# Performance work log

Measured on AMD Instinct MI355X. Metric: run time of the kernel, lower is better.

## Reference

```python
import jax, jax.numpy as jnp
import numpy as np

KERNEL_LAM = 0.1


def setup_inputs() -> dict:
    key = jax.random.key(0)
    k1, k2, k3, k4 = jax.random.split(key, 4)
    B, H, L, C = 4, 1024, 4096, 1
    u = jax.random.normal(k1, (B, H, L), dtype=jnp.float32)
    kernel = jax.random.normal(k2, (C, H, 2 * L), dtype=jnp.float32) * 0.002
    D = jax.random.normal(k3, (C, H), dtype=jnp.float32)
    W = jax.random.normal(k4, (2 * H, C * H), dtype=jnp.float32) * (1.0 / np.sqrt(C * H))
    b = jnp.zeros((2 * H,), dtype=jnp.float32)
    return {"u": u, "kernel": kernel, "D": D, "W": W, "b": b}


def reference(u, kernel, D, W, b):
    B, H, L = u.shape
    n = 2 * L  # FFT length (kernel is length 2L)
    # soft-threshold the kernel
    k = jax.nn.relu(jnp.abs(kernel) - KERNEL_LAM) * jnp.sign(kernel)  # (C,H,2L)
    # FFT-based long convolution (flashfftconv equivalent): causal conv, take first L
    kf = jnp.fft.rfft(k, n=n)                       # (C,H,n//2+1)
    uf = jnp.fft.rfft(u, n=n)                       # (B,H,n//2+1)
    y = jnp.fft.irfft(uf[:, None] * kf[None], n=n)[..., :L]  # (B,C,H,L)
    # skip connection with D
    y = y + jnp.einsum('bhl,ch->bchl', u, D)
    # (B, C*H, L)
    y = y.reshape(B, -1, L)
    y = jax.nn.silu(y)
    # GLU projection over channel dim
    z = jnp.swapaxes(y, -1, -2) @ W.T + b           # (B,L,2H)
    a, g = jnp.split(z, 2, axis=-1)
    out = a * jax.nn.sigmoid(g)                     # (B,L,H)
    return jnp.swapaxes(out, -1, -2)                # (B,H,L)
```

## Files before the change

kernel.cpp:

```cpp
#include <hip/hip_runtime.h>
#include <stdint.h>

#define HD   1024
#define LD   4096
#define BATCH 4
#define KLEN 8192
#define LAM  0.1f
#define TAP_CAP 65536

typedef __attribute__((ext_vector_type(8))) short short8x;
typedef __attribute__((ext_vector_type(4))) float float4x;

struct Tap { int hd; float v; };

__device__ inline unsigned short f2bf(float x) {
    union { float f; uint32_t u; } v; v.f = x;
    uint32_t u = v.u;
    u += 0x7fffu + ((u >> 16) & 1u);
    return (unsigned short)(u >> 16);
}

__device__ inline void gload16(const void* g, void* l) {
    __builtin_amdgcn_global_load_lds(
        (const __attribute__((address_space(1))) void*)g,
        (__attribute__((address_space(3))) void*)l,
        16, 0, 0);
}

__device__ inline float silu_f(float x) { return x / (1.0f + __expf(-x)); }

__global__ void k_prep(const float* __restrict__ kern, int* __restrict__ ntaps,
                       Tap* __restrict__ taps,
                       const float* __restrict__ W, unsigned short* __restrict__ Wbf) {
    if (blockIdx.x < 1024) {
        int i = blockIdx.x * 256 + threadIdx.x;
        const float4* w4 = (const float4*)W;
        float4 a = w4[i * 2], b = w4[i * 2 + 1];
        short8x o;
        o[0] = (short)f2bf(a.x); o[1] = (short)f2bf(a.y);
        o[2] = (short)f2bf(a.z); o[3] = (short)f2bf(a.w);
        o[4] = (short)f2bf(b.x); o[5] = (short)f2bf(b.y);
        o[6] = (short)f2bf(b.z); o[7] = (short)f2bf(b.w);
        *(short8x*)(Wbf + (int64_t)i * 8) = o;
        return;
    }
    int bid = blockIdx.x - 1024;
    const float4* k4 = (const float4*)kern;
    int64_t total4 = (int64_t)HD * KLEN / 4;
    int64_t stride = (int64_t)2048 * 256;
    for (int64_t i = (int64_t)bid * 256 + threadIdx.x; i < total4; i += stride) {
        float4 v = k4[i];
        float vals[4] = {v.x, v.y, v.z, v.w};
#pragma unroll
        for (int j = 0; j < 4; j++) {
            float a = fabsf(vals[j]) - LAM;
            if (a > 0.0f) {
                int e = (int)(i * 4 + j);
                int slot = atomicAdd(ntaps, 1);
                if (slot < TAP_CAP) { taps[slot].hd = e; taps[slot].v = copysignf(a, vals[j]); }
            }
        }
    }
}

__global__ void k_conv(const float* __restrict__ u, const float* __restrict__ Dv,
                       const int* __restrict__ ntaps_p, const Tap* __restrict__ taps,
                       float* __restrict__ yfull) {
    int nt = *ntaps_p;
    if (nt == 0) return;
    nt = min(nt, TAP_CAP);
    int64_t total = (int64_t)BATCH * HD * LD;
    int64_t stride = (int64_t)gridDim.x * blockDim.x;
    for (int64_t i = (int64_t)blockIdx.x * blockDim.x + threadIdx.x; i < total; i += stride) {
        int t = (int)(i & (LD - 1));
        int64_t bh = i >> 12;
        int h = (int)(bh & (HD - 1));
        float acc = u[i] * Dv[h];
        for (int j = 0; j < nt; j++) {
            int hd = taps[j].hd;
            if ((hd >> 13) != h) continue;
            int d = hd & (KLEN - 1);
            int s;
            if (d <= t) s = t - d;
            else { s = t - d + KLEN; if (s >= LD) continue; }
            acc += taps[j].v * u[(bh << 12) + s];
        }
        yfull[i] = acc;
    }
}

__global__ __launch_bounds__(256) void k_vt(const float* __restrict__ u,
                                            const float* __restrict__ Dv,
                                            const float* __restrict__ yfull,
                                            const int* __restrict__ ntaps_p,
                                            unsigned short* __restrict__ Vt) {
    __shared__ float T[64 * 65];
    int nt = *ntaps_p;
    int lt = blockIdx.x * 64;
    int ht = blockIdx.y * 64;
    int b  = blockIdx.z;
    int tid = threadIdx.x;
    int lq = tid & 15;
    int hh = tid >> 4;
#pragma unroll
    for (int r = 0; r < 4; r++) {
        int h = hh + r * 16;
        int hg = ht + h;
        int64_t base = ((int64_t)b * HD + hg) * LD + lt + lq * 4;
        float4 v;
        if (nt == 0) {
            v = *(const float4*)(u + base);
            float d = Dv[hg];
            v.x *= d; v.y *= d; v.z *= d; v.w *= d;
        } else {
            v = *(const float4*)(yfull + base);
        }
        int p = h * 65 + lq * 4;
        T[p]     = silu_f(v.x);
        T[p + 1] = silu_f(v.y);
        T[p + 2] = silu_f(v.z);
        T[p + 3] = silu_f(v.w);
    }
    __syncthreads();
    int h8 = (tid & 7) * 8;
    int nb = tid >> 3;
#pragma unroll
    for (int p = 0; p < 2; p++) {
        int nl = nb + p * 32;
        short8x o;
#pragma unroll
        for (int j = 0; j < 8; j++) o[j] = (short)f2bf(T[(h8 + j) * 65 + nl]);
        int64_t n = (int64_t)b * LD + lt + nl;
        *(short8x*)(Vt + n * HD + ht + h8) = o;
    }
}

__global__ __launch_bounds__(256, 2) void k_gemm(const unsigned short* __restrict__ Wbf,
                                                 const unsigned short* __restrict__ Vt,
                                                 const float* __restrict__ bvec,
                                                 float* __restrict__ out) {
    __shared__ unsigned short smem[12288];
    int f   = blockIdx.x;
    int xcd = f & 7;
    int s   = f >> 3;
    int ngrp = xcd * 16 + (s & 15);
    int mgrp = s >> 4;
    int m0 = mgrp * 128;
    int n0 = ngrp * 128;
    int tid = threadIdx.x;

    const unsigned short* gsrc[6];
    unsigned short* ldst[6];
#pragma unroll
    for (int i = 0; i < 6; i++) {
        int c = tid + i * 256;
        ldst[i] = smem + c * 8;
        if (c < 1024) {
            int r = c >> 2, slot = c & 3;
            int kg = slot ^ (r & 3);
            int grow = (r < 128) ? (m0 + r) : (1024 + m0 + (r - 128));
            gsrc[i] = Wbf + (int64_t)grow * HD + kg * 8;
        } else {
            int cc = c - 1024;
            int col = cc >> 2, slot = cc & 3;
            int kg = slot ^ (col & 3);
            gsrc[i] = Vt + (int64_t)(n0 + col) * HD + kg * 8;
        }
    }

    int lane = tid & 63;
    int wid  = tid >> 6;
    int wm = wid >> 1, wn = wid & 1;
    int l15 = lane & 15, quad = lane >> 4;
    int kq = quad ^ (l15 & 3);

    int aoff[4], goff[4], boff[4];
#pragma unroll
    for (int i = 0; i < 4; i++) {
        int ra = wm * 64 + i * 16 + l15;
        aoff[i] = ra * 32 + kq * 8;
        goff[i] = (128 + ra) * 32 + kq * 8;
        int cb = wn * 64 + i * 16 + l15;
        boff[i] = 8192 + cb * 32 + kq * 8;
    }

    float4x acca[4][4], accg[4][4];
#pragma unroll
    for (int i = 0; i < 4; i++)
#pragma unroll
        for (int j = 0; j < 4; j++) {
            acca[i][j] = (float4x){0.f, 0.f, 0.f, 0.f};
            accg[i][j] = (float4x){0.f, 0.f, 0.f, 0.f};
        }

    for (int kt = 0; kt < 32; kt++) {
#pragma unroll
        for (int i = 0; i < 6; i++) gload16(gsrc[i], ldst[i]);
#pragma unroll
        for (int i = 0; i < 6; i++) gsrc[i] += 32;
        __syncthreads();
        short8x af[4], gf[4], bf[4];
#pragma unroll
        for (int i = 0; i < 4; i++) {
            af[i] = *(const short8x*)(smem + aoff[i]);
            gf[i] = *(const short8x*)(smem + goff[i]);
            bf[i] = *(const short8x*)(smem + boff[i]);
        }
#pragma unroll
        for (int i = 0; i < 4; i++)
#pragma unroll
            for (int j = 0; j < 4; j++) {
                acca[i][j] = __builtin_amdgcn_mfma_f32_16x16x32_bf16(af[i], bf[j], acca[i][j], 0, 0, 0);
                accg[i][j] = __builtin_amdgcn_mfma_f32_16x16x32_bf16(gf[i], bf[j], accg[i][j], 0, 0, 0);
            }
        __syncthreads();
    }

    int b = n0 >> 12;
#pragma unroll
    for (int i = 0; i < 4; i++) {
        int h = m0 + wm * 64 + i * 16 + quad * 4;
        float ba[4], bg[4];
#pragma unroll
        for (int r = 0; r < 4; r++) { ba[r] = bvec[h + r]; bg[r] = bvec[1024 + h + r]; }
#pragma unroll
        for (int j = 0; j < 4; j++) {
            int n = n0 + wn * 64 + j * 16 + l15;
            int l = n & (LD - 1);
            float* op = out + ((int64_t)b * HD + h) * LD + l;
#pragma unroll
            for (int r = 0; r < 4; r++) {
                float av = acca[i][j][r] + ba[r];
                float gv = accg[i][j][r] + bg[r];
                op[(int64_t)r * LD] = av / (1.0f + __expf(-gv));
            }
        }
    }
}

extern "C" void kernel_launch(void* const* d_in, const int* in_sizes, int n_in,
                              void* d_out, int out_size, void* d_ws, size_t ws_size,
                              hipStream_t stream) {
    const float* u    = (const float*)d_in[0];
    const float* kern = (const float*)d_in[1];
    const float* Dv   = (const float*)d_in[2];
    const float* W    = (const float*)d_in[3];
    const float* bv   = (const float*)d_in[4];
    float* out = (float*)d_out;

    char* ws = (char*)d_ws;
    int* ntaps = (int*)ws;
    Tap* taps  = (Tap*)(ws + 256);
    unsigned short* Wbf = (unsigned short*)(ws + (1 << 20));
    unsigned short* Vt  = (unsigned short*)(ws + (8 << 20));
    float* yfull = (float*)(ws + (40 << 20));

    hipMemsetAsync(ntaps, 0, 256, stream);
    hipLaunchKernelGGL(k_prep, dim3(3072),      dim3(256), 0, stream, kern, ntaps, taps, W, (unsigned short*)Wbf);
    hipLaunchKernelGGL(k_conv, dim3(512),       dim3(256), 0, stream, u, Dv, ntaps, taps, yfull);
    hipLaunchKernelGGL(k_vt,   dim3(64, 16, 4), dim3(256), 0, stream, u, Dv, yfull, ntaps, Vt);
    hipLaunchKernelGGL(k_gemm, dim3(1024),      dim3(256), 0, stream, Wbf, Vt, bv, out);
}
```

Before: 233.8 us.

## Load GEMM MFMA operands directly from global memory instead of LDS staging

The GLU GEMM kernel stops staging W and V tiles through shared memory with global_load_lds and barriers. Each lane now reads its bf16 fragments straight from global memory, and the k-loop is fully unrolled. The block-to-tile mapping also changes from an XCD-aware swizzle to a simple m-fastest order. This removes the LDS round trip and the barrier synchronisation, at the cost of redundant global and L2 traffic, since tiles are no longer shared across waves, and of possibly worse latency hiding. The yfull workspace offset is moved as well.

```diff
diff --git a/kernel.cpp b/kernel.cpp
--- a/kernel.cpp
+++ b/kernel.cpp
@@ -18,13 +18,6 @@
     uint32_t u = v.u;
     u += 0x7fffu + ((u >> 16) & 1u);
     return (unsigned short)(u >> 16);
-}
-
-__device__ inline void gload16(const void* g, void* l) {
-    __builtin_amdgcn_global_load_lds(
-        (const __attribute__((address_space(1))) void*)g,
-        (__attribute__((address_space(3))) void*)l,
-        16, 0, 0);
 }
 
 __device__ inline float silu_f(float x) { return x / (1.0f + __expf(-x)); }
@@ -139,49 +132,26 @@
                                                  const unsigned short* __restrict__ Vt,
                                                  const float* __restrict__ bvec,
                                                  float* __restrict__ out) {
-    __shared__ unsigned short smem[12288];
-    int f   = blockIdx.x;
-    int xcd = f & 7;
-    int s   = f >> 3;
-    int ngrp = xcd * 16 + (s & 15);
-    int mgrp = s >> 4;
+    int mgrp = blockIdx.x & 7;
+    int ngrp = blockIdx.x >> 3;
     int m0 = mgrp * 128;
     int n0 = ngrp * 128;
     int tid = threadIdx.x;
-
-    const unsigned short* gsrc[6];
-    unsigned short* ldst[6];
-#pragma unroll
-    for (int i = 0; i < 6; i++) {
-        int c = tid + i * 256;
-        ldst[i] = smem + c * 8;
-        if (c < 1024) {
-            int r = c >> 2, slot = c & 3;
-            int kg = slot ^ (r & 3);
-            int grow = (r < 128) ? (m0 + r) : (1024 + m0 + (r - 128));
-            gsrc[i] = Wbf + (int64_t)grow * HD + kg * 8;
-        } else {
-            int cc = c - 1024;
-            int col = cc >> 2, slot = cc & 3;
-            int kg = slot ^ (col & 3);
-            gsrc[i] = Vt + (int64_t)(n0 + col) * HD + kg * 8;
-        }
-    }
-
     int lane = tid & 63;
     int wid  = tid >> 6;
     int wm = wid >> 1, wn = wid & 1;
     int l15 = lane & 15, quad = lane >> 4;
-    int kq = quad ^ (l15 & 3);
-
-    int aoff[4], goff[4], boff[4];
+
+    const short8x* pa[4];
+    const short8x* pg[4];
+    const short8x* pb[4];
 #pragma unroll
     for (int i = 0; i < 4; i++) {
-        int ra = wm * 64 + i * 16 + l15;
-        aoff[i] = ra * 32 + kq * 8;
-        goff[i] = (128 + ra) * 32 + kq * 8;
-        int cb = wn * 64 + i * 16 + l15;
-        boff[i] = 8192 + cb * 32 + kq * 8;
+        int ra = m0 + wm * 64 + i * 16 + l15;
+        pa[i] = (const short8x*)(Wbf + (uint32_t)ra * 1024u + quad * 8);
+        pg[i] = (const short8x*)(Wbf + (uint32_t)(ra + 1024) * 1024u + quad * 8);
+        int nb = n0 + wn * 64 + i * 16 + l15;
+        pb[i] = (const short8x*)(Vt + (uint32_t)nb * 1024u + quad * 8);
     }
 
     float4x acca[4][4], accg[4][4];
@@ -193,18 +163,14 @@
             accg[i][j] = (float4x){0.f, 0.f, 0.f, 0.f};
         }
 
+#pragma unroll
     for (int kt = 0; kt < 32; kt++) {
-#pragma unroll
-        for (int i = 0; i < 6; i++) gload16(gsrc[i], ldst[i]);
-#pragma unroll
-        for (int i = 0; i < 6; i++) gsrc[i] += 32;
-        __syncthreads();
         short8x af[4], gf[4], bf[4];
 #pragma unroll
         for (int i = 0; i < 4; i++) {
-            af[i] = *(const short8x*)(smem + aoff[i]);
-            gf[i] = *(const short8x*)(smem + goff[i]);
-            bf[i] = *(const short8x*)(smem + boff[i]);
+            af[i] = pa[i][kt * 4];
+            gf[i] = pg[i][kt * 4];
+            bf[i] = pb[i][kt * 4];
         }
 #pragma unroll
         for (int i = 0; i < 4; i++)
@@ -213,7 +179,6 @@
                 acca[i][j] = __builtin_amdgcn_mfma_f32_16x16x32_bf16(af[i], bf[j], acca[i][j], 0, 0, 0);
                 accg[i][j] = __builtin_amdgcn_mfma_f32_16x16x32_bf16(gf[i], bf[j], accg[i][j], 0, 0, 0);
             }
-        __syncthreads();
     }
 
     int b = n0 >> 12;
@@ -253,10 +218,10 @@
     Tap* taps  = (Tap*)(ws + 256);
     unsigned short* Wbf = (unsigned short*)(ws + (1 << 20));
     unsigned short* Vt  = (unsigned short*)(ws + (8 << 20));
-    float* yfull = (float*)(ws + (40 << 20));
+    float* yfull = (float*)(ws + (48 << 20));
 
     hipMemsetAsync(ntaps, 0, 256, stream);
-    hipLaunchKernelGGL(k_prep, dim3(3072),      dim3(256), 0, stream, kern, ntaps, taps, W, (unsigned short*)Wbf);
+    hipLaunchKernelGGL(k_prep, dim3(3072),      dim3(256), 0, stream, kern, ntaps, taps, W, Wbf);
     hipLaunchKernelGGL(k_conv, dim3(512),       dim3(256), 0, stream, u, Dv, ntaps, taps, yfull);
     hipLaunchKernelGGL(k_vt,   dim3(64, 16, 4), dim3(256), 0, stream, u, Dv, yfull, ntaps, Vt);
     hipLaunchKernelGGL(k_gemm, dim3(1024),      dim3(256), 0, stream, Wbf, Vt, bv, out);
```

After: 336.6 us. 1.44x slower.

## Fuse sparse tap convolution into transpose kernel and deepen GEMM K-tile

Applied to the files above, without the earlier changes.

Removes the separate k_conv kernel and its full fp32 yfull buffer, folding the sparse tap convolution directly into the k_vt transpose/SiLU kernel. This avoids an extra write and read of the activation tensor plus a kernel launch. The GEMM now stages a K-tile of 64 instead of 32, using 8-way XOR swizzling and halving the number of barrier iterations. Its grid becomes a plain 2D mapping without the XCD-aware remap. The larger LDS footprint (48KB) may reduce occupancy, and dropping the XCD remap may hurt L2 locality.

```diff
diff --git a/kernel.cpp b/kernel.cpp
--- a/kernel.cpp
+++ b/kernel.cpp
@@ -63,36 +63,10 @@
     }
 }
 
-__global__ void k_conv(const float* __restrict__ u, const float* __restrict__ Dv,
-                       const int* __restrict__ ntaps_p, const Tap* __restrict__ taps,
-                       float* __restrict__ yfull) {
-    int nt = *ntaps_p;
-    if (nt == 0) return;
-    nt = min(nt, TAP_CAP);
-    int64_t total = (int64_t)BATCH * HD * LD;
-    int64_t stride = (int64_t)gridDim.x * blockDim.x;
-    for (int64_t i = (int64_t)blockIdx.x * blockDim.x + threadIdx.x; i < total; i += stride) {
-        int t = (int)(i & (LD - 1));
-        int64_t bh = i >> 12;
-        int h = (int)(bh & (HD - 1));
-        float acc = u[i] * Dv[h];
-        for (int j = 0; j < nt; j++) {
-            int hd = taps[j].hd;
-            if ((hd >> 13) != h) continue;
-            int d = hd & (KLEN - 1);
-            int s;
-            if (d <= t) s = t - d;
-            else { s = t - d + KLEN; if (s >= LD) continue; }
-            acc += taps[j].v * u[(bh << 12) + s];
-        }
-        yfull[i] = acc;
-    }
-}
-
 __global__ __launch_bounds__(256) void k_vt(const float* __restrict__ u,
                                             const float* __restrict__ Dv,
-                                            const float* __restrict__ yfull,
                                             const int* __restrict__ ntaps_p,
+                                            const Tap* __restrict__ taps,
                                             unsigned short* __restrict__ Vt) {
     __shared__ float T[64 * 65];
     int nt = *ntaps_p;
@@ -107,13 +81,26 @@
         int h = hh + r * 16;
         int hg = ht + h;
         int64_t base = ((int64_t)b * HD + hg) * LD + lt + lq * 4;
-        float4 v;
-        if (nt == 0) {
-            v = *(const float4*)(u + base);
-            float d = Dv[hg];
-            v.x *= d; v.y *= d; v.z *= d; v.w *= d;
-        } else {
-            v = *(const float4*)(yfull + base);
+        float4 v = *(const float4*)(u + base);
+        float d = Dv[hg];
+        v.x *= d; v.y *= d; v.z *= d; v.w *= d;
+        if (nt != 0) {
+            int ncl = min(nt, TAP_CAP);
+            float acc[4] = {v.x, v.y, v.z, v.w};
+            const float* ub = u + ((int64_t)b * HD + hg) * LD;
+            for (int j = 0; j < ncl; j++) {
+                int hd = taps[j].hd;
+                if ((hd >> 13) != hg) continue;
+                int dly = hd & (KLEN - 1);
+#pragma unroll
+                for (int e = 0; e < 4; e++) {
+                    int t = lt + lq * 4 + e;
+                    int s = t - dly;
+                    if (s < 0) s += KLEN;
+                    if (s < LD) acc[e] += taps[j].v * ub[s];
+                }
+            }
+            v.x = acc[0]; v.y = acc[1]; v.z = acc[2]; v.w = acc[3];
         }
         int p = h * 65 + lq * 4;
         T[p]     = silu_f(v.x);
@@ -139,31 +126,26 @@
                                                  const unsigned short* __restrict__ Vt,
                                                  const float* __restrict__ bvec,
                                                  float* __restrict__ out) {
-    __shared__ unsigned short smem[12288];
-    int f   = blockIdx.x;
-    int xcd = f & 7;
-    int s   = f >> 3;
-    int ngrp = xcd * 16 + (s & 15);
-    int mgrp = s >> 4;
-    int m0 = mgrp * 128;
-    int n0 = ngrp * 128;
+    __shared__ unsigned short smem[24576];
+    int m0 = blockIdx.x * 128;
+    int n0 = blockIdx.y * 128;
     int tid = threadIdx.x;
 
-    const unsigned short* gsrc[6];
-    unsigned short* ldst[6];
-#pragma unroll
-    for (int i = 0; i < 6; i++) {
+    const unsigned short* gsrc[12];
+    unsigned short* ldst[12];
+#pragma unroll
+    for (int i = 0; i < 12; i++) {
         int c = tid + i * 256;
         ldst[i] = smem + c * 8;
-        if (c < 1024) {
-            int r = c >> 2, slot = c & 3;
-            int kg = slot ^ (r & 3);
+        if (c < 2048) {
+            int r = c >> 3, s = c & 7;
+            int kg = s ^ (r & 7);
             int grow = (r < 128) ? (m0 + r) : (1024 + m0 + (r - 128));
             gsrc[i] = Wbf + (int64_t)grow * HD + kg * 8;
         } else {
-            int cc = c - 1024;
-            int col = cc >> 2, slot = cc & 3;
-            int kg = slot ^ (col & 3);
+            int cc = c - 2048;
+            int col = cc >> 3, s = cc & 7;
+            int kg = s ^ (col & 7);
             gsrc[i] = Vt + (int64_t)(n0 + col) * HD + kg * 8;
         }
     }
@@ -172,16 +154,16 @@
     int wid  = tid >> 6;
     int wm = wid >> 1, wn = wid & 1;
     int l15 = lane & 15, quad = lane >> 4;
-    int kq = quad ^ (l15 & 3);
-
-    int aoff[4], goff[4], boff[4];
+    int xr = l15 & 7;
+
+    int rba[4], rbg[4], rbb[4];
 #pragma unroll
     for (int i = 0; i < 4; i++) {
         int ra = wm * 64 + i * 16 + l15;
-        aoff[i] = ra * 32 + kq * 8;
-        goff[i] = (128 + ra) * 32 + kq * 8;
+        rba[i] = ra * 64;
+        rbg[i] = (128 + ra) * 64;
         int cb = wn * 64 + i * 16 + l15;
-        boff[i] = 8192 + cb * 32 + kq * 8;
+        rbb[i] = 16384 + cb * 64;
     }
 
     float4x acca[4][4], accg[4][4];
@@ -193,26 +175,30 @@
             accg[i][j] = (float4x){0.f, 0.f, 0.f, 0.f};
         }
 
-    for (int kt = 0; kt < 32; kt++) {
-#pragma unroll
-        for (int i = 0; i < 6; i++) gload16(gsrc[i], ldst[i]);
-#pragma unroll
-        for (int i = 0; i < 6; i++) gsrc[i] += 32;
+    for (int kt = 0; kt < 16; kt++) {
+#pragma unroll
+        for (int i = 0; i < 12; i++) gload16(gsrc[i], ldst[i]);
+#pragma unroll
+        for (int i = 0; i < 12; i++) gsrc[i] += 64;
         __syncthreads();
-        short8x af[4], gf[4], bf[4];
-#pragma unroll
-        for (int i = 0; i < 4; i++) {
-            af[i] = *(const short8x*)(smem + aoff[i]);
-            gf[i] = *(const short8x*)(smem + goff[i]);
-            bf[i] = *(const short8x*)(smem + boff[i]);
-        }
-#pragma unroll
-        for (int i = 0; i < 4; i++)
-#pragma unroll
-            for (int j = 0; j < 4; j++) {
-                acca[i][j] = __builtin_amdgcn_mfma_f32_16x16x32_bf16(af[i], bf[j], acca[i][j], 0, 0, 0);
-                accg[i][j] = __builtin_amdgcn_mfma_f32_16x16x32_bf16(gf[i], bf[j], accg[i][j], 0, 0, 0);
-            }
+#pragma unroll
+        for (int ks = 0; ks < 2; ks++) {
+            int off = ((ks * 4 + quad) ^ xr) * 8;
+            short8x af[4], gf[4], bf[4];
+#pragma unroll
+            for (int i = 0; i < 4; i++) {
+                af[i] = *(const short8x*)(smem + rba[i] + off);
+                gf[i] = *(const short8x*)(smem + rbg[i] + off);
+                bf[i] = *(const short8x*)(smem + rbb[i] + off);
+            }
+#pragma unroll
+            for (int i = 0; i < 4; i++)
+#pragma unroll
+                for (int j = 0; j < 4; j++) {
+                    acca[i][j] = __builtin_amdgcn_mfma_f32_16x16x32_bf16(af[i], bf[j], acca[i][j], 0, 0, 0);
+                    accg[i][j] = __builtin_amdgcn_mfma_f32_16x16x32_bf16(gf[i], bf[j], accg[i][j], 0, 0, 0);
+                }
+        }
         __syncthreads();
     }
 
@@ -253,11 +239,9 @@
     Tap* taps  = (Tap*)(ws + 256);
     unsigned short* Wbf = (unsigned short*)(ws + (1 << 20));
     unsigned short* Vt  = (unsigned short*)(ws + (8 << 20));
-    float* yfull = (float*)(ws + (40 << 20));
 
     hipMemsetAsync(ntaps, 0, 256, stream);
-    hipLaunchKernelGGL(k_prep, dim3(3072),      dim3(256), 0, stream, kern, ntaps, taps, W, (unsigned short*)Wbf);
-    hipLaunchKernelGGL(k_conv, dim3(512),       dim3(256), 0, stream, u, Dv, ntaps, taps, yfull);
-    hipLaunchKernelGGL(k_vt,   dim3(64, 16, 4), dim3(256), 0, stream, u, Dv, yfull, ntaps, Vt);
-    hipLaunchKernelGGL(k_gemm, dim3(1024),      dim3(256), 0, stream, Wbf, Vt, bv, out);
-}
+    hipLaunchKernelGGL(k_prep, dim3(3072),      dim3(256), 0, stream, kern, ntaps, taps, W, Wbf);
+    hipLaunchKernelGGL(k_vt,   dim3(64, 16, 4), dim3(256), 0, stream, u, Dv, ntaps, taps, Vt);
+    hipLaunchKernelGGL(k_gemm, dim3(8, 128),    dim3(256), 0, stream, Wbf, Vt, bv, out);
+}
```

After: 219.4 us. 1.07x faster.
